# Kernel optimization log

Hardware: AMD Instinct MI355X
Metric: run time of the kernel (lower is better)

The kernel has to match this reference:

```python
import jax, jax.numpy as jnp
import numpy as np

M0, M1 = 32, 16          # multiplicities of 0e (scalars) and 1o (vectors)
FEAT = M0 + 3 * M1       # 80
WNUM = M0*M0 + M1*M1 + M0*M1 + M1*M0  # 2304 per-edge TP weights
N_NODES, N_EDGES, N_RBF, HID = 10000, 160000, 50, 64
EPS = 1e-5
INV_SQRT3 = 1.0 / np.sqrt(3.0)
# per-path normalization: 1/sqrt(num_paths_to_output * mul_in)
A_P1 = 1.0 / np.sqrt(2.0 * M0)   # 0e x 0e -> 0e
A_P4 = 1.0 / np.sqrt(2.0 * M1)   # 1o x 1o -> 0e
A_P2 = 1.0 / np.sqrt(2.0 * M1)   # 1o x 0e -> 1o
A_P3 = 1.0 / np.sqrt(2.0 * M0)   # 0e x 1o -> 1o


def setup_inputs() -> dict:
    key = jax.random.key(0)
    ks = jax.random.split(key, 12)
    def lin(k, fi, fo):
        return jax.random.normal(k, (fi, fo), jnp.float32) / np.sqrt(fi)
    return dict(
        h=jax.random.normal(ks[0], (N_NODES, FEAT), jnp.float32),
        edge_index=jax.random.randint(ks[1], (2, N_EDGES), 0, N_NODES),
        edge_sh=jax.random.normal(ks[2], (N_EDGES, 4), jnp.float32),
        edge_features=jax.random.normal(ks[3], (N_EDGES, N_RBF), jnp.float32),
        W1e=lin(ks[4], N_RBF, HID), b1e=jnp.zeros(HID, jnp.float32),
        W2e=lin(ks[5], HID, HID), b2e=jnp.zeros(HID, jnp.float32),
        W3e=lin(ks[6], HID, WNUM) * 0.1, b3e=jnp.zeros(WNUM, jnp.float32),
        A0=jax.random.normal(ks[7], (M0, M0), jnp.float32),
        A1p=jax.random.normal(ks[8], (M1, M1), jnp.float32),
        bn_w0=jnp.ones(M0, jnp.float32), bn_b0=jnp.zeros(M0, jnp.float32),
        bn_w1=jnp.ones(M1, jnp.float32),
    )


def _forward(h, edge_index, edge_sh, edge_features,
             W1e, b1e, W2e, b2e, W3e, b3e, A0, A1p, bn_w0, bn_b0, bn_w1):
    N = h.shape[0]
    E = edge_sh.shape[0]
    src, dst = edge_index[0], edge_index[1]

    # ---- edge MLP -> per-edge tensor-product weights [E, WNUM] ----
    w = jax.nn.silu(edge_features @ W1e + b1e)
    w = jax.nn.silu(w @ W2e + b2e)
    w = w @ W3e + b3e
    o1 = M0 * M0
    o2 = o1 + M1 * M1
    o3 = o2 + M0 * M1
    w1 = w[:, :o1].reshape(E, M0, M0)     # 0e x 0e -> 0e
    w2 = w[:, o1:o2].reshape(E, M1, M1)   # 1o x 0e -> 1o
    w3 = w[:, o2:o3].reshape(E, M0, M1)   # 0e x 1o -> 1o
    w4 = w[:, o3:].reshape(E, M1, M0)     # 1o x 1o -> 0e

    # ---- gather source node features ----
    s0 = h[src, :M0]                         # [E, M0]
    s1 = h[src, M0:].reshape(E, M1, 3)       # [E, M1, 3]
    y0 = edge_sh[:, 0]                       # [E]
    y1 = edge_sh[:, 1:4]                     # [E, 3]

    # ---- fully connected tensor product with per-edge weights ----
    # scalar output: 0e x 0e -> 0e  and  1o x 1o -> 0e (dot / sqrt(3))
    dot11 = jnp.einsum('eui,ei->eu', s1, y1) * INV_SQRT3      # [E, M1]
    m0 = (A_P1 * jnp.einsum('eu,euw->ew', s0 * y0[:, None], w1)
          + A_P4 * jnp.einsum('eu,euw->ew', dot11, w4))       # [E, M0]
    # vector output: 1o x 0e -> 1o  and  0e x 1o -> 1o
    m1 = (A_P2 * jnp.einsum('eui,euw->ewi', s1 * y0[:, None, None], w2)
          + A_P3 * jnp.einsum('eu,ei,euw->ewi', s0, y1, w3))  # [E, M1, 3]
    messages = jnp.concatenate([m0, m1.reshape(E, 3 * M1)], axis=1)  # [E, FEAT]

    # ---- scatter-mean aggregation to destination nodes ----
    agg = jax.ops.segment_sum(messages, dst, num_segments=N)
    cnt = jax.ops.segment_sum(jnp.ones((E,), messages.dtype), dst, num_segments=N)
    agg = agg / jnp.maximum(cnt, 1.0)[:, None]

    # ---- equivariant self-interaction (per-l linear mixing) ----
    self0 = (h[:, :M0] @ A0) / np.sqrt(M0)
    h1 = h[:, M0:].reshape(N, M1, 3)
    self1 = jnp.einsum('nui,uw->nwi', h1, A1p) / np.sqrt(M1)
    out = agg + jnp.concatenate([self0, self1.reshape(N, 3 * M1)], axis=1)

    # ---- equivariant batch norm (layer mode) ----
    x0 = out[:, :M0]
    x1 = out[:, M0:].reshape(N, M1, 3)
    mu = x0.mean(axis=0)
    var = x0.var(axis=0)
    x0n = (x0 - mu) * jax.lax.rsqrt(var + EPS) * bn_w0 + bn_b0
    nrm2 = (x1 ** 2).sum(axis=-1).mean(axis=0)               # [M1]
    x1n = x1 * (jax.lax.rsqrt(nrm2 + EPS) * bn_w1)[None, :, None]
    out = jnp.concatenate([x0n, x1n.reshape(N, 3 * M1)], axis=1)

    # ---- residual (irreps_in == irreps_out) ----
    return out + h


def reference(h, edge_index, edge_sh, edge_features,
              W1e, b1e, W2e, b2e, W3e, b3e, A0, A1p, bn_w0, bn_b0, bn_w1):
    return _forward(h, edge_index, edge_sh, edge_features,
                    W1e, b1e, W2e, b2e, W3e, b3e, A0, A1p, bn_w0, bn_b0, bn_w1)
```

## Files before the change

### kernel.cpp

```cpp
#include <hip/hip_runtime.h>
#include <math.h>

#define NN 10000
#define NE 160000
#define NRBF 50
#define WNUM 2304
#define EPSV 1e-5f

#define A_P1 0.125f
#define A_P2 0.17677669529663687f
#define A_P3 0.125f
#define A_P4 0.17677669529663687f
#define INV_SQRT3 0.5773502691896258f
#define INV_SQRT_M0 0.17677669529663687f
#define INV_SQRT_M1 0.25f

typedef __attribute__((ext_vector_type(8))) short bf16x8;
typedef __attribute__((ext_vector_type(4))) float f32x4;
typedef __attribute__((ext_vector_type(4))) int i32x4;

#define MFMA16(a, b, c) __builtin_amdgcn_mfma_f32_16x16x32_bf16(a, b, c, 0, 0, 0)

__device__ __forceinline__ short f2bf(float x) {
  unsigned u = __float_as_uint(x);
  unsigned r = (u + 0x7fffu + ((u >> 16) & 1u)) >> 16;
  return (short)r;
}

__global__ void prep_weights(const float* __restrict__ W1, const float* __restrict__ W2,
                             const float* __restrict__ W3, short* __restrict__ W1P,
                             short* __restrict__ W2P, short* __restrict__ W3P) {
  int s = blockIdx.x * 256 + threadIdx.x;
  if (s < WNUM * 64) {
    int t = s >> 10, r = s & 1023;
    int ch = r >> 9, l = (r >> 3) & 63, kk = r & 7;
    int row = t * 16 + (l & 15);
    int k = ((l >> 4) << 3) + (ch << 5) + kk;
    W3P[s] = f2bf(W3[k * WNUM + row]);
  } else if (s < WNUM * 64 + 4096) {
    int s2 = s - WNUM * 64;
    int t = s2 >> 10, r = s2 & 1023;
    int ch = r >> 9, l = (r >> 3) & 63, kk = r & 7;
    int row = t * 16 + (l & 15);
    int k = ((l >> 4) << 3) + (ch << 5) + kk;
    W1P[s2] = f2bf(k < NRBF ? W1[k * 64 + row] : 0.f);
  } else if (s < WNUM * 64 + 8192) {
    int s2 = s - WNUM * 64 - 4096;
    int t = s2 >> 10, r = s2 & 1023;
    int ch = r >> 9, l = (r >> 3) & 63, kk = r & 7;
    int row = t * 16 + (l & 15);
    int k = ((l >> 4) << 3) + (ch << 5) + kk;
    W2P[s2] = f2bf(W2[k * 64 + row]);
  }
}

#define TILE4(T, ...)                                               \
  {                                                                 \
    const short* _wb = W3P + ((T) << 10) + (l << 3);                \
    bf16x8 _B0 = *(const bf16x8*)_wb;                               \
    bf16x8 _B1 = *(const bf16x8*)(_wb + 512);                       \
    float _bias = b3[((T) << 4) + lr];                              \
    _Pragma("unroll")                                               \
    for (int g = 0; g < 4; ++g) {                                   \
      f32x4 _d = {_bias, _bias, _bias, _bias};                      \
      _d = MFMA16(a0g[g], _B0, _d);                                 \
      f32x4 v = MFMA16(a1g[g], _B1, _d);                            \
      __VA_ARGS__                                                   \
    }                                                               \
  }

__global__ __launch_bounds__(256, 3) void edge_kernel(
    const float* __restrict__ h, const int* __restrict__ eidx,
    const float* __restrict__ esh, const float* __restrict__ ef,
    const short* __restrict__ W1P, const float* __restrict__ b1,
    const short* __restrict__ W2P, const float* __restrict__ b2,
    const short* __restrict__ W3P, const float* __restrict__ b3,
    float* __restrict__ agg, float* __restrict__ cnt) {
  __shared__ short buf0[64 * 72];
  __shared__ short h1s[64 * 72];
  __shared__ float coef[6144];
  __shared__ float y0s[64], y1s[192];
  __shared__ float b1s[64], b2s[64];
  __shared__ int dsts[64];

  const int tid = threadIdx.x;
  const int e0 = blockIdx.x * 64;

  for (int idx = tid; idx < 64 * 64; idx += 256) {
    int e = idx >> 6, k = idx & 63;
    float v = (k < NRBF) ? ef[(long)(e0 + e) * NRBF + k] : 0.f;
    buf0[e * 72 + k] = f2bf(v);
  }
  if (tid < 64) { b1s[tid] = b1[tid]; b2s[tid] = b2[tid]; }
  {
    int e = tid >> 2, q = tid & 3;
    int ge = e0 + e;
    int src = eidx[ge];
    float y0 = esh[ge * 4 + 0];
    float y1x = esh[ge * 4 + 1], y1y = esh[ge * 4 + 2], y1z = esh[ge * 4 + 3];
    const float* hs = h + (long)src * 80;
    for (int u = q; u < 32; u += 4) coef[u * 64 + e] = A_P3 * hs[u];
    for (int u = q; u < 16; u += 4) {
      float sx = hs[32 + u * 3], sy = hs[33 + u * 3], sz = hs[34 + u * 3];
      coef[2048 + (0 * 16 + u) * 64 + e] = A_P2 * sx;
      coef[2048 + (1 * 16 + u) * 64 + e] = A_P2 * sy;
      coef[2048 + (2 * 16 + u) * 64 + e] = A_P2 * sz;
      coef[5120 + u * 64 + e] = A_P4 * INV_SQRT3 * (sx * y1x + sy * y1y + sz * y1z);
    }
    if (q == 0) {
      y0s[e] = y0;
      y1s[e] = y1x; y1s[64 + e] = y1y; y1s[128 + e] = y1z;
      dsts[e] = eidx[NE + ge];
    }
  }
  __syncthreads();

  const int wid = tid >> 6, l = tid & 63;
  const int lr = l & 15, lg = l >> 4;
  const int g16 = lg * 4;

  {
    const int er = wid * 16;
    bf16x8 a0 = *(const bf16x8*)&buf0[(er + lr) * 72 + lg * 8];
    bf16x8 a1 = *(const bf16x8*)&buf0[(er + lr) * 72 + 32 + lg * 8];
#pragma unroll
    for (int jt = 0; jt < 4; ++jt) {
      const short* wb = W1P + (jt << 10) + (l << 3);
      bf16x8 b0 = *(const bf16x8*)wb;
      bf16x8 b1f = *(const bf16x8*)(wb + 512);
      float bias = b1s[jt * 16 + lr];
      f32x4 d = {bias, bias, bias, bias};
      d = MFMA16(a0, b0, d);
      d = MFMA16(a1, b1f, d);
#pragma unroll
      for (int r = 0; r < 4; ++r) {
        float x = d[r];
        x = x / (1.f + __expf(-x));
        h1s[(er + lg * 4 + r) * 72 + jt * 16 + lr] = f2bf(x);
      }
    }
  }
  __syncthreads();

  {
    const int er = wid * 16;
    bf16x8 a0 = *(const bf16x8*)&h1s[(er + lr) * 72 + lg * 8];
    bf16x8 a1 = *(const bf16x8*)&h1s[(er + lr) * 72 + 32 + lg * 8];
#pragma unroll
    for (int jt = 0; jt < 4; ++jt) {
      const short* wb = W2P + (jt << 10) + (l << 3);
      bf16x8 b0 = *(const bf16x8*)wb;
      bf16x8 b1f = *(const bf16x8*)(wb + 512);
      float bias = b2s[jt * 16 + lr];
      f32x4 d = {bias, bias, bias, bias};
      d = MFMA16(a0, b0, d);
      d = MFMA16(a1, b1f, d);
#pragma unroll
      for (int r = 0; r < 4; ++r) {
        float x = d[r];
        x = x / (1.f + __expf(-x));
        buf0[(er + lg * 4 + r) * 72 + jt * 16 + lr] = f2bf(x);
      }
    }
  }
  __syncthreads();

  bf16x8 a0g[4], a1g[4];
#pragma unroll
  for (int g = 0; g < 4; ++g) {
    a0g[g] = *(const bf16x8*)&buf0[(g * 16 + lr) * 72 + lg * 8];
    a1g[g] = *(const bf16x8*)&buf0[(g * 16 + lr) * 72 + 32 + lg * 8];
  }

  f32x4 s0[4], s1[4], mx[4], my[4], mz[4];
#pragma unroll
  for (int g = 0; g < 4; ++g) {
    s0[g] = (f32x4){0, 0, 0, 0}; s1[g] = (f32x4){0, 0, 0, 0};
    mx[g] = (f32x4){0, 0, 0, 0}; my[g] = (f32x4){0, 0, 0, 0};
    mz[g] = (f32x4){0, 0, 0, 0};
  }

  if (wid == 0) {
#pragma unroll 1
    for (int p = 0; p < 18; ++p) {
      TILE4(2 * p, {
        f32x4 c = *(const f32x4*)&coef[p * 64 + g * 16 + g16];
        _Pragma("unroll") for (int r = 0; r < 4; ++r) s0[g][r] += c[r] * v[r];
      });
      TILE4(2 * p + 1, {
        f32x4 c = *(const f32x4*)&coef[p * 64 + g * 16 + g16];
        _Pragma("unroll") for (int r = 0; r < 4; ++r) s1[g][r] += c[r] * v[r];
      });
    }
#pragma unroll
    for (int g = 0; g < 4; ++g) {
      f32x4 y0v = *(const f32x4*)&y0s[g * 16 + g16];
#pragma unroll
      for (int r = 0; r < 4; ++r) { s0[g][r] *= y0v[r]; s1[g][r] *= y0v[r]; }
    }
  } else if (wid == 1) {
#pragma unroll 1
    for (int p = 18; p < 32; ++p) {
      TILE4(2 * p, {
        f32x4 c = *(const f32x4*)&coef[p * 64 + g * 16 + g16];
        _Pragma("unroll") for (int r = 0; r < 4; ++r) s0[g][r] += c[r] * v[r];
      });
      TILE4(2 * p + 1, {
        f32x4 c = *(const f32x4*)&coef[p * 64 + g * 16 + g16];
        _Pragma("unroll") for (int r = 0; r < 4; ++r) s1[g][r] += c[r] * v[r];
      });
    }
#pragma unroll 2
    for (int u = 0; u < 8; ++u) {
      TILE4(64 + u, {
        f32x4 cx = *(const f32x4*)&coef[2048 + (0 * 16 + u) * 64 + g * 16 + g16];
        f32x4 cy = *(const f32x4*)&coef[2048 + (1 * 16 + u) * 64 + g * 16 + g16];
        f32x4 cz = *(const f32x4*)&coef[2048 + (2 * 16 + u) * 64 + g * 16 + g16];
        _Pragma("unroll") for (int r = 0; r < 4; ++r) {
          mx[g][r] += cx[r] * v[r];
          my[g][r] += cy[r] * v[r];
          mz[g][r] += cz[r] * v[r];
        }
      });
    }
#pragma unroll
    for (int g = 0; g < 4; ++g) {
      f32x4 y0v = *(const f32x4*)&y0s[g * 16 + g16];
#pragma unroll
      for (int r = 0; r < 4; ++r) {
        s0[g][r] *= y0v[r]; s1[g][r] *= y0v[r];
        mx[g][r] *= y0v[r]; my[g][r] *= y0v[r]; mz[g][r] *= y0v[r];
      }
    }
  } else if (wid == 2) {
#pragma unroll 2
    for (int u = 8; u < 16; ++u) {
      TILE4(64 + u, {
        f32x4 cx = *(const f32x4*)&coef[2048 + (0 * 16 + u) * 64 + g * 16 + g16];
        f32x4 cy = *(const f32x4*)&coef[2048 + (1 * 16 + u) * 64 + g * 16 + g16];
        f32x4 cz = *(const f32x4*)&coef[2048 + (2 * 16 + u) * 64 + g * 16 + g16];
        _Pragma("unroll") for (int r = 0; r < 4; ++r) {
          mx[g][r] += cx[r] * v[r];
          my[g][r] += cy[r] * v[r];
          mz[g][r] += cz[r] * v[r];
        }
      });
    }
#pragma unroll
    for (int g = 0; g < 4; ++g) {
      f32x4 y0v = *(const f32x4*)&y0s[g * 16 + g16];
#pragma unroll
      for (int r = 0; r < 4; ++r) {
        mx[g][r] *= y0v[r]; my[g][r] *= y0v[r]; mz[g][r] *= y0v[r];
      }
    }
#pragma unroll 2
    for (int u = 0; u < 28; ++u) {
      TILE4(80 + u, {
        f32x4 c = *(const f32x4*)&coef[u * 64 + g * 16 + g16];
        _Pragma("unroll") for (int r = 0; r < 4; ++r) s0[g][r] += c[r] * v[r];
      });
    }
#pragma unroll
    for (int g = 0; g < 4; ++g) {
      f32x4 yx = *(const f32x4*)&y1s[g * 16 + g16];
      f32x4 yy = *(const f32x4*)&y1s[64 + g * 16 + g16];
      f32x4 yz = *(const f32x4*)&y1s[128 + g * 16 + g16];
#pragma unroll
      for (int r = 0; r < 4; ++r) {
        mx[g][r] += yx[r] * s0[g][r];
        my[g][r] += yy[r] * s0[g][r];
        mz[g][r] += yz[r] * s0[g][r];
      }
      s0[g] = (f32x4){0, 0, 0, 0};
    }
  } else {
    {
      f32x4 yx[4], yy[4], yz[4];
#pragma unroll
      for (int g = 0; g < 4; ++g) {
        yx[g] = *(const f32x4*)&y1s[g * 16 + g16];
        yy[g] = *(const f32x4*)&y1s[64 + g * 16 + g16];
        yz[g] = *(const f32x4*)&y1s[128 + g * 16 + g16];
      }
#pragma unroll 2
      for (int u = 28; u < 32; ++u) {
        TILE4(80 + u, {
          f32x4 c = *(const f32x4*)&coef[u * 64 + g * 16 + g16];
          _Pragma("unroll") for (int r = 0; r < 4; ++r) {
            float t = c[r] * v[r];
            mx[g][r] += yx[g][r] * t;
            my[g][r] += yy[g][r] * t;
            mz[g][r] += yz[g][r] * t;
          }
        });
      }
    }
#pragma unroll 1
    for (int p = 0; p < 16; ++p) {
      TILE4(112 + 2 * p, {
        f32x4 c = *(const f32x4*)&coef[5120 + p * 64 + g * 16 + g16];
        _Pragma("unroll") for (int r = 0; r < 4; ++r) s0[g][r] += c[r] * v[r];
      });
      TILE4(113 + 2 * p, {
        f32x4 c = *(const f32x4*)&coef[5120 + p * 64 + g * 16 + g16];
        _Pragma("unroll") for (int r = 0; r < 4; ++r) s1[g][r] += c[r] * v[r];
      });
    }
  }

  if (tid < 64) atomicAdd(cnt + dsts[tid], 1.0f);

#define STORE_G(G, BASE)                                \
  {                                                     \
    float* p = coef + (BASE) + l * 24;                  \
    *(f32x4*)(p + 0) = s0[G];  *(f32x4*)(p + 4) = s1[G];\
    *(f32x4*)(p + 8) = mx[G];  *(f32x4*)(p + 12) = my[G];\
    *(f32x4*)(p + 16) = mz[G];                          \
  }
#define ADD_G(G, BASE)                                                   \
  {                                                                      \
    const float* p = coef + (BASE) + l * 24;                             \
    f32x4 t0 = *(const f32x4*)(p + 0), t1 = *(const f32x4*)(p + 4);      \
    f32x4 t2 = *(const f32x4*)(p + 8), t3_ = *(const f32x4*)(p + 12);    \
    f32x4 t4 = *(const f32x4*)(p + 16);                                  \
    _Pragma("unroll") for (int r = 0; r < 4; ++r) {                      \
      s0[G][r] += t0[r]; s1[G][r] += t1[r]; mx[G][r] += t2[r];           \
      my[G][r] += t3_[r]; mz[G][r] += t4[r];                             \
    }                                                                    \
  }

  __syncthreads();
  if (wid == 1) { STORE_G(0, 0); STORE_G(1, 1536); }
  if (wid == 3) { STORE_G(0, 3072); STORE_G(1, 4608); }
  __syncthreads();
  if (wid == 0) { ADD_G(0, 0); ADD_G(1, 1536); }
  if (wid == 2) { ADD_G(0, 3072); ADD_G(1, 4608); }
  __syncthreads();
  if (wid == 1) { STORE_G(2, 0); STORE_G(3, 1536); }
  if (wid == 3) { STORE_G(2, 3072); STORE_G(3, 4608); }
  __syncthreads();
  if (wid == 0) { ADD_G(2, 0); ADD_G(3, 1536); }
  if (wid == 2) { ADD_G(2, 3072); ADD_G(3, 4608); }
  __syncthreads();
  if (wid == 2) { STORE_G(0, 0); STORE_G(1, 1536); STORE_G(2, 3072); STORE_G(3, 4608); }
  __syncthreads();
  if (wid == 0) {
    ADD_G(0, 0); ADD_G(1, 1536); ADD_G(2, 3072); ADD_G(3, 4608);
#pragma unroll
    for (int g = 0; g < 4; ++g) {
      i32x4 dd = *(const i32x4*)&dsts[g * 16 + g16];
#pragma unroll
      for (int r = 0; r < 4; ++r) {
        float* base = agg + (long)dd[r] * 80;
        atomicAdd(base + lr, s0[g][r]);
        atomicAdd(base + 16 + lr, s1[g][r]);
        atomicAdd(base + 32 + lr * 3 + 0, mx[g][r]);
        atomicAdd(base + 32 + lr * 3 + 1, my[g][r]);
        atomicAdd(base + 32 + lr * 3 + 2, mz[g][r]);
      }
    }
  }
#undef STORE_G
#undef ADD_G
}

__global__ __launch_bounds__(256) void node_a(
    const float* __restrict__ h, const float* __restrict__ A0,
    const float* __restrict__ A1p, const float* __restrict__ agg,
    const float* __restrict__ cnt, float* __restrict__ outpre,
    float* __restrict__ stats) {
  __shared__ float redw[4][80];
  const int tid = threadIdx.x;
  const int wid = tid >> 6, l = tid & 63;
  const int n = blockIdx.x * 256 + tid;
  float x0[32], x1[48];
#pragma unroll
  for (int w = 0; w < 32; w++) x0[w] = 0.f;
#pragma unroll
  for (int c = 0; c < 48; c++) x1[c] = 0.f;
  if (n < NN) {
    const float* hr = h + (long)n * 80;
    const float* ar = agg + (long)n * 80;
    float inv = 1.f / fmaxf(cnt[n], 1.f);
#pragma unroll 1
    for (int u = 0; u < 32; u++) {
      float hu = hr[u];
#pragma unroll
      for (int w = 0; w < 32; w++) x0[w] += hu * A0[u * 32 + w];
    }
#pragma unroll
    for (int w = 0; w < 32; w++) x0[w] = x0[w] * INV_SQRT_M0 + ar[w] * inv;
#pragma unroll 1
    for (int u = 0; u < 16; u++) {
      float a = hr[32 + u * 3], b_ = hr[33 + u * 3], c_ = hr[34 + u * 3];
#pragma unroll
      for (int w = 0; w < 16; w++) {
        float Aw = A1p[u * 16 + w];
        x1[w * 3 + 0] += a * Aw;
        x1[w * 3 + 1] += b_ * Aw;
        x1[w * 3 + 2] += c_ * Aw;
      }
    }
#pragma unroll
    for (int c = 0; c < 48; c++) x1[c] = x1[c] * INV_SQRT_M1 + ar[32 + c] * inv;
    float* opr = outpre + (long)n * 80;
#pragma unroll
    for (int w = 0; w < 32; w++) opr[w] = x0[w];
#pragma unroll
    for (int c = 0; c < 48; c++) opr[32 + c] = x1[c];
  }
#pragma unroll 1
  for (int c = 0; c < 32; ++c) {
    float s = x0[c];
#pragma unroll
    for (int m = 32; m >= 1; m >>= 1) s += __shfl_xor(s, m, 64);
    if (l == 0) redw[wid][c] = s;
  }
#pragma unroll 1
  for (int c = 0; c < 32; ++c) {
    float v = x0[c];
    float s = v * v;
#pragma unroll
    for (int m = 32; m >= 1; m >>= 1) s += __shfl_xor(s, m, 64);
    if (l == 0) redw[wid][32 + c] = s;
  }
#pragma unroll 1
  for (int u = 0; u < 16; ++u) {
    float s = x1[u * 3] * x1[u * 3] + x1[u * 3 + 1] * x1[u * 3 + 1] +
              x1[u * 3 + 2] * x1[u * 3 + 2];
#pragma unroll
    for (int m = 32; m >= 1; m >>= 1) s += __shfl_xor(s, m, 64);
    if (l == 0) redw[wid][64 + u] = s;
  }
  __syncthreads();
  if (tid < 80)
    atomicAdd(&stats[tid],
              redw[0][tid] + redw[1][tid] + redw[2][tid] + redw[3][tid]);
}

__global__ void node_b(const float* __restrict__ outpre, const float* __restrict__ stats,
                       const float* __restrict__ bnw0, const float* __restrict__ bnb0,
                       const float* __restrict__ bnw1, const float* __restrict__ h,
                       float* __restrict__ out) {
  int idx = blockIdx.x * 256 + threadIdx.x;
  if (idx >= NN * 80) return;
  int c = idx % 80;
  float v = outpre[idx];
  const float invN = 1.f / NN;
  float o;
  if (c < 32) {
    float mu = stats[c] * invN;
    float var = stats[32 + c] * invN - mu * mu;
    o = (v - mu) * rsqrtf(var + EPSV) * bnw0[c] + bnb0[c];
  } else {
    int u = (c - 32) / 3;
    float nr = stats[64 + u] * invN;
    o = v * rsqrtf(nr + EPSV) * bnw1[u];
  }
  out[idx] = o + h[idx];
}

extern "C" void kernel_launch(void* const* d_in, const int* in_sizes, int n_in,
                              void* d_out, int out_size, void* d_ws, size_t ws_size,
                              hipStream_t stream) {
  const float* h    = (const float*)d_in[0];
  const int*   eidx = (const int*)d_in[1];
  const float* esh  = (const float*)d_in[2];
  const float* ef   = (const float*)d_in[3];
  const float* W1   = (const float*)d_in[4];
  const float* b1   = (const float*)d_in[5];
  const float* W2   = (const float*)d_in[6];
  const float* b2   = (const float*)d_in[7];
  const float* W3   = (const float*)d_in[8];
  const float* b3   = (const float*)d_in[9];
  const float* A0   = (const float*)d_in[10];
  const float* A1p  = (const float*)d_in[11];
  const float* bnw0 = (const float*)d_in[12];
  const float* bnb0 = (const float*)d_in[13];
  const float* bnw1 = (const float*)d_in[14];
  float* out = (float*)d_out;

  float* ws = (float*)d_ws;
  float* agg    = ws;
  float* cnt    = ws + 800000;
  float* stats  = ws + 810000;
  float* outpre = ws + 810080;
  short* W3P    = (short*)(ws + 1610080);
  short* W1P    = W3P + WNUM * 64;
  short* W2P    = W1P + 4096;

  hipMemsetAsync(agg, 0, (size_t)810080 * sizeof(float), stream);

  prep_weights<<<(WNUM * 64 + 8192 + 255) / 256, 256, 0, stream>>>(W1, W2, W3, W1P,
                                                                   W2P, W3P);
  edge_kernel<<<NE / 64, 256, 0, stream>>>(h, eidx, esh, ef, W1P, b1, W2P, b2, W3P, b3,
                                           agg, cnt);
  node_a<<<(NN + 255) / 256, 256, 0, stream>>>(h, A0, A1p, agg, cnt, outpre, stats);
  node_b<<<(NN * 80 + 255) / 256, 256, 0, stream>>>(outpre, stats, bnw0, bnb0, bnw1, h,
                                                    out);
}
```

Baseline: 235.4 us.

## Replace atomic scatter aggregation with CSR-sorted per-node gather of edge messages

Builds a CSR index of edges by destination (count, scan, place kernels), has the edge kernel write per-edge messages densely to a workspace buffer instead of issuing float atomics, and adds a node_gather kernel that sums each node's messages and divides by degree. This aims to remove the contention and serialization of per-edge float atomicAdds into agg. It costs extra kernel launches, a single-block scan, a 51 MB message write and reread, and it falls back to the atomic path if the workspace is too small.

```diff
diff --git a/kernel.cpp b/kernel.cpp
--- a/kernel.cpp
+++ b/kernel.cpp
@@ -54,6 +54,51 @@
   }
 }
 
+__global__ void edge_count(const int* __restrict__ eidx, int* __restrict__ deg) {
+  int e = blockIdx.x * 256 + threadIdx.x;
+  if (e < NE) atomicAdd(&deg[eidx[NE + e]], 1);
+}
+
+__global__ __launch_bounds__(256) void scan_deg(const int* __restrict__ deg,
+                                                int* __restrict__ offs) {
+  __shared__ int chunk[10240];
+  __shared__ int part[256];
+  const int tid = threadIdx.x;
+  const int base = tid * 40;
+  int s = 0;
+  for (int i = 0; i < 40; i++) {
+    int idx = base + i;
+    int v = (idx < NN) ? deg[idx] : 0;
+    chunk[base + i] = s;
+    s += v;
+  }
+  const int tot = s;
+  part[tid] = s;
+  __syncthreads();
+  for (int d = 1; d < 256; d <<= 1) {
+    int v = (tid >= d) ? part[tid - d] : 0;
+    __syncthreads();
+    if (tid >= d) part[tid] += v;
+    __syncthreads();
+  }
+  int excl = part[tid] - tot;
+  for (int i = 0; i < 40; i++) {
+    int idx = base + i;
+    if (idx < NN) offs[idx] = chunk[base + i] + excl;
+  }
+  if (tid == 255) offs[NN] = part[255];
+}
+
+__global__ void edge_place(const int* __restrict__ eidx, const int* __restrict__ offs,
+                           int* __restrict__ slot, int* __restrict__ csr) {
+  int e = blockIdx.x * 256 + threadIdx.x;
+  if (e < NE) {
+    int d = eidx[NE + e];
+    int pos = offs[d] + atomicAdd(&slot[d], 1);
+    csr[pos] = e;
+  }
+}
+
 #define TILE4(T, ...)                                               \
   {                                                                 \
     const short* _wb = W3P + ((T) << 10) + (l << 3);                \
@@ -75,7 +120,7 @@
     const short* __restrict__ W1P, const float* __restrict__ b1,
     const short* __restrict__ W2P, const float* __restrict__ b2,
     const short* __restrict__ W3P, const float* __restrict__ b3,
-    float* __restrict__ agg, float* __restrict__ cnt) {
+    float* __restrict__ agg, float* __restrict__ msg, int use_csr) {
   __shared__ short buf0[64 * 72];
   __shared__ short h1s[64 * 72];
   __shared__ float coef[6144];
@@ -309,8 +354,6 @@
     }
   }
 
-  if (tid < 64) atomicAdd(cnt + dsts[tid], 1.0f);
-
 #define STORE_G(G, BASE)                                \
   {                                                     \
     float* p = coef + (BASE) + l * 24;                  \
@@ -345,31 +388,76 @@
   __syncthreads();
   if (wid == 2) { STORE_G(0, 0); STORE_G(1, 1536); STORE_G(2, 3072); STORE_G(3, 4608); }
   __syncthreads();
-  if (wid == 0) {
-    ADD_G(0, 0); ADD_G(1, 1536); ADD_G(2, 3072); ADD_G(3, 4608);
-#pragma unroll
-    for (int g = 0; g < 4; ++g) {
-      i32x4 dd = *(const i32x4*)&dsts[g * 16 + g16];
-#pragma unroll
-      for (int r = 0; r < 4; ++r) {
-        float* base = agg + (long)dd[r] * 80;
-        atomicAdd(base + lr, s0[g][r]);
-        atomicAdd(base + 16 + lr, s1[g][r]);
-        atomicAdd(base + 32 + lr * 3 + 0, mx[g][r]);
-        atomicAdd(base + 32 + lr * 3 + 1, my[g][r]);
-        atomicAdd(base + 32 + lr * 3 + 2, mz[g][r]);
+
+  if (use_csr) {
+    if (wid == 0) {
+      ADD_G(0, 0); ADD_G(1, 1536); ADD_G(2, 3072); ADD_G(3, 4608);
+#pragma unroll
+      for (int g = 0; g < 4; ++g) {
+#pragma unroll
+        for (int r = 0; r < 4; ++r) {
+          float* mrow = coef + (g * 16 + g16 + r) * 80;
+          mrow[lr] = s0[g][r];
+          mrow[16 + lr] = s1[g][r];
+          mrow[32 + lr * 3 + 0] = mx[g][r];
+          mrow[32 + lr * 3 + 1] = my[g][r];
+          mrow[32 + lr * 3 + 2] = mz[g][r];
+        }
+      }
+    }
+    __syncthreads();
+    float* mp = msg + (long)e0 * 80;
+#pragma unroll
+    for (int q = 0; q < 5; ++q) {
+      *(f32x4*)&mp[tid * 20 + q * 4] = *(const f32x4*)&coef[tid * 20 + q * 4];
+    }
+  } else {
+    if (wid == 0) {
+      ADD_G(0, 0); ADD_G(1, 1536); ADD_G(2, 3072); ADD_G(3, 4608);
+#pragma unroll
+      for (int g = 0; g < 4; ++g) {
+        i32x4 dd = *(const i32x4*)&dsts[g * 16 + g16];
+#pragma unroll
+        for (int r = 0; r < 4; ++r) {
+          float* base = agg + (long)dd[r] * 80;
+          atomicAdd(base + lr, s0[g][r]);
+          atomicAdd(base + 16 + lr, s1[g][r]);
+          atomicAdd(base + 32 + lr * 3 + 0, mx[g][r]);
+          atomicAdd(base + 32 + lr * 3 + 1, my[g][r]);
+          atomicAdd(base + 32 + lr * 3 + 2, mz[g][r]);
+        }
       }
     }
   }
 #undef STORE_G
 #undef ADD_G
+}
+
+__global__ __launch_bounds__(256) void node_gather(
+    const float* __restrict__ msg, const int* __restrict__ csr,
+    const int* __restrict__ offs, const int* __restrict__ deg,
+    float* __restrict__ agg) {
+  const int wid = threadIdx.x >> 6, l = threadIdx.x & 63;
+  const int n = blockIdx.x * 4 + wid;
+  if (n >= NN) return;
+  const int s = offs[n];
+  const int ep = deg[n];
+  float a0 = 0.f, a1 = 0.f;
+  for (int i = 0; i < ep; ++i) {
+    long rb = (long)csr[s + i] * 80;
+    a0 += msg[rb + l];
+    if (l < 16) a1 += msg[rb + 64 + l];
+  }
+  float inv = 1.f / fmaxf((float)ep, 1.f);
+  agg[(long)n * 80 + l] = a0 * inv;
+  if (l < 16) agg[(long)n * 80 + 64 + l] = a1 * inv;
 }
 
 __global__ __launch_bounds__(256) void node_a(
     const float* __restrict__ h, const float* __restrict__ A0,
     const float* __restrict__ A1p, const float* __restrict__ agg,
-    const float* __restrict__ cnt, float* __restrict__ outpre,
-    float* __restrict__ stats) {
+    const int* __restrict__ deg, float* __restrict__ outpre,
+    float* __restrict__ stats, int mean_done) {
   __shared__ float redw[4][80];
   const int tid = threadIdx.x;
   const int wid = tid >> 6, l = tid & 63;
@@ -382,7 +470,7 @@
   if (n < NN) {
     const float* hr = h + (long)n * 80;
     const float* ar = agg + (long)n * 80;
-    float inv = 1.f / fmaxf(cnt[n], 1.f);
+    float inv = mean_done ? 1.f : 1.f / fmaxf((float)deg[n], 1.f);
 #pragma unroll 1
     for (int u = 0; u < 32; u++) {
       float hu = hr[u];
@@ -483,20 +571,37 @@
 
   float* ws = (float*)d_ws;
   float* agg    = ws;
-  float* cnt    = ws + 800000;
-  float* stats  = ws + 810000;
-  float* outpre = ws + 810080;
-  short* W3P    = (short*)(ws + 1610080);
+  float* stats  = ws + 800000;
+  float* outpre = ws + 800080;
+  short* W3P    = (short*)(ws + 1600080);
   short* W1P    = W3P + WNUM * 64;
   short* W2P    = W1P + 4096;
-
-  hipMemsetAsync(agg, 0, (size_t)810080 * sizeof(float), stream);
+  int*   deg    = (int*)(ws + 1677904);
+  int*   slot   = deg + 10000;
+  int*   offs   = slot + 10000;
+  int*   csr    = offs + 10001;
+  float* msg    = ws + 1677904 + 190004;
+
+  const size_t need = (size_t)(1677904 + 190004 + 12800000) * 4;
+  const int use_csr = (ws_size >= need) ? 1 : 0;
+
+  hipMemsetAsync(agg, 0, (size_t)800080 * sizeof(float), stream);
+  hipMemsetAsync(deg, 0, (size_t)20000 * sizeof(int), stream);
 
   prep_weights<<<(WNUM * 64 + 8192 + 255) / 256, 256, 0, stream>>>(W1, W2, W3, W1P,
                                                                    W2P, W3P);
+  edge_count<<<(NE + 255) / 256, 256, 0, stream>>>(eidx, deg);
+  if (use_csr) {
+    scan_deg<<<1, 256, 0, stream>>>(deg, offs);
+    edge_place<<<(NE + 255) / 256, 256, 0, stream>>>(eidx, offs, slot, csr);
+  }
   edge_kernel<<<NE / 64, 256, 0, stream>>>(h, eidx, esh, ef, W1P, b1, W2P, b2, W3P, b3,
-                                           agg, cnt);
-  node_a<<<(NN + 255) / 256, 256, 0, stream>>>(h, A0, A1p, agg, cnt, outpre, stats);
+                                           agg, msg, use_csr);
+  if (use_csr) {
+    node_gather<<<(NN + 3) / 4, 256, 0, stream>>>(msg, csr, offs, deg, agg);
+  }
+  node_a<<<(NN + 255) / 256, 256, 0, stream>>>(h, A0, A1p, agg, deg, outpre, stats,
+                                               use_csr);
   node_b<<<(NN * 80 + 255) / 256, 256, 0, stream>>>(outpre, stats, bnw0, bnb0, bnw1, h,
                                                     out);
 }
```

Measured after the change: 268.7 us. +14.1%, slower.
